# Performance work log

Measured on AMD Instinct MI355X. Metric: run time of the kernel, lower is better.

## Reference

```python
import jax, jax.numpy as jnp
import numpy as np

NEG_INF = -1e30


def setup_inputs() -> dict:
    key = jax.random.key(0)
    kx, km, kq, kk, kv, ko = jax.random.split(key, 6)
    B, D, L = 2, 1024, 2048
    H, DK = 16, 64
    x = jax.random.normal(kx, (B, D, L), dtype=jnp.float32)
    mask = (jax.random.uniform(km, (B, L)) < 0.9).astype(jnp.float32)
    # per-head projection weights, stacked: (H, D, DK); output proj (D, H*DK)==(D, D)
    sq = 1.0 / np.sqrt(D)
    Wq = jax.random.normal(kq, (H, D, DK), dtype=jnp.float32) * sq
    Wk = jax.random.normal(kk, (H, D, DK), dtype=jnp.float32) * sq
    Wv = jax.random.normal(kv, (H, D, DK), dtype=jnp.float32) * sq
    Wo = jax.random.normal(ko, (D, H * DK), dtype=jnp.float32) * sq
    return {"x": x, "mask": mask, "Wq": Wq, "Wk": Wk, "Wv": Wv, "Wo": Wo}


def reference(x, mask, Wq, Wk, Wv, Wo):
    # x: (B, D, L); original transposes to (B, L, D)
    B, D, L = x.shape
    H, _, DK = Wq.shape
    xt = jnp.transpose(x, (0, 2, 1))  # (B, L, D)
    q = jnp.einsum('bld,hdk->bhlk', xt, Wq)
    k = jnp.einsum('bld,hdk->bhlk', xt, Wk)
    v = jnp.einsum('bld,hdk->bhlk', xt, Wv)
    scores = jnp.einsum('bhlk,bhmk->bhlm', q, k) * (1.0 / np.sqrt(DK))
    # masked log-softmax over keys (hmask), squad-style: mask*logit + (1-mask)*-1e30
    hmask = mask[:, None, None, :]  # (B,1,1,Lk)
    masked = hmask * scores + (1.0 - hmask) * NEG_INF
    logp = jax.nn.log_softmax(masked, axis=-1)
    # second softmax over the log-probs, then multiplicative vmask on query dim
    p = jax.nn.softmax(logp, axis=-1) * mask[:, None, :, None]
    heads = jnp.einsum('bhlm,bhmk->bhlk', p, v)  # (B,H,L,DK)
    head = jnp.transpose(heads, (0, 2, 1, 3)).reshape(B, L, H * DK)
    out = jnp.einsum('ble,de->bld', head, Wo)  # matmul(head, Wo) with Wo (D, H*DK)... 
    # NOTE: torch.matmul(head, Wo) treats Wo as (H*DK_in, D_out) only if square; here
    # Wo is (D, H*DK) with D == H*DK, and torch contracts head's last dim with Wo's FIRST dim:
    out = head @ Wo  # (B, L, H*DK) @ (D, H*DK) requires D==H*DK; contracts dim 0 of Wo
    return jnp.transpose(out, (0, 2, 1))  # (B, D, L)


if __name__ == "__main__":
    print(reference(**setup_inputs()).shape)
```

## Files before the change

### kernel.cpp

```cpp
#include <hip/hip_runtime.h>
#include <hip/hip_bf16.h>

typedef unsigned short u16;
typedef unsigned int u32;
typedef unsigned long long u64;
typedef short s8v __attribute__((ext_vector_type(8)));
typedef short s4v __attribute__((ext_vector_type(4)));
typedef __bf16 bfv8 __attribute__((ext_vector_type(8)));
typedef float f4 __attribute__((ext_vector_type(4)));

static constexpr int B = 2, D = 1024, L = 2048, H = 16, DK = 64, E = 1024;
static constexpr float QSCALE = 0.125f * 1.44269504088896340736f;
static constexpr float SMB = -16.0f;
static constexpr float MASKB = -12000.0f;

#define DEV __device__ __forceinline__

DEV u16 f2bf(float f) {
  unsigned int u = __float_as_uint(f);
  u += 0x7FFFu + ((u >> 16) & 1u);
  return (u16)(u >> 16);
}
DEV float fexp2(float x) { return __builtin_amdgcn_exp2f(x); }
DEV u32 pkbf(float a, float b) {
  __hip_bfloat162 h = __float22bfloat162_rn(float2{a, b});
  u32 r;
  __builtin_memcpy(&r, &h, 4);
  return r;
}

DEV f4 mfma16(s4v a, s4v b, f4 c) {
  return __builtin_amdgcn_mfma_f32_16x16x16bf16_1k(a, b, c, 0, 0, 0);
}

#define GLD_LDS16(gp, lp)                                                     \
  __builtin_amdgcn_global_load_lds(                                           \
      (const __attribute__((address_space(1))) void*)(gp),                    \
      (__attribute__((address_space(3))) void*)(lp), 16, 0, 0)

__global__ __launch_bounds__(256) void k_prep(
    const float* __restrict__ x, const float* __restrict__ Wq,
    const float* __restrict__ Wk, const float* __restrict__ Wv,
    const float* __restrict__ Wo, u16* __restrict__ xt, u16* __restrict__ Wt,
    u16* __restrict__ WoT) {
  __shared__ u16 t[64][67];
  const int tid = threadIdx.x;
  const int g = blockIdx.x;
  const float* src;
  u16* dst;
  int sld, dld;
  if (g < 1024) {
    const int b = g >> 9, dt = (g >> 5) & 15, lt = g & 31;
    src = x + ((size_t)b * D + dt * 64) * L + lt * 64;
    sld = L;
    dst = xt + ((size_t)b * L + lt * 64) * D + dt * 64;
    dld = D;
  } else if (g < 1792) {
    const int u = g - 1024;
    const int w = u >> 8, h = (u >> 4) & 15, dt = u & 15;
    const float* Ws = (w == 0) ? Wq : ((w == 1) ? Wk : Wv);
    src = Ws + ((size_t)h * D + dt * 64) * DK;
    sld = DK;
    dst = Wt + ((size_t)(w * H + h) * DK) * D + dt * 64;
    dld = D;
  } else {
    const int v = g - 1792;
    const int et = v >> 4, dt = v & 15;
    src = Wo + ((size_t)et * 64) * D + dt * 64;
    sld = D;
    dst = WoT + ((size_t)dt * 64) * E + et * 64;
    dld = E;
  }
  const int r = tid >> 2, c16 = (tid & 3) * 16;
#pragma unroll
  for (int j = 0; j < 16; j += 4) {
    const f4 v4 = *(const f4*)(src + (size_t)r * sld + c16 + j);
    t[r][c16 + j]     = f2bf(v4[0]);
    t[r][c16 + j + 1] = f2bf(v4[1]);
    t[r][c16 + j + 2] = f2bf(v4[2]);
    t[r][c16 + j + 3] = f2bf(v4[3]);
  }
  __syncthreads();
  s8v o0, o1;
#pragma unroll
  for (int i = 0; i < 8; ++i) {
    o0[i] = (short)t[c16 + i][r];
    o1[i] = (short)t[c16 + 8 + i][r];
  }
  *(s8v*)(dst + (size_t)r * dld + c16)     = o0;
  *(s8v*)(dst + (size_t)r * dld + c16 + 8) = o1;
}

template <int AR>
DEV void gemm_tile(const u16* __restrict__ A, const u16* __restrict__ Bt,
                   int arow0, int brow0, u16* As, u16* Bs,
                   f4 (&acc)[AR / 32][4]) {
  const int tid = threadIdx.x;
  const int wid = tid >> 6, lane = tid & 63;
  const int q = lane >> 4, ln = lane & 15;
  const int wr = wid >> 1, wc = wid & 1;
  const int lrow = lane >> 3;
  const int lc = (lane & 7) ^ lrow;
  const int f0 = (q ^ (ln & 7)) * 8;
  const int f1 = ((q + 4) ^ (ln & 7)) * 8;
  constexpr int MT = AR / 32;

  for (int k0 = 0; k0 < 1024; k0 += 64) {
    __syncthreads();
#pragma unroll
    for (int j = 0; j < AR / 32; ++j) {
      const int rb = wid * (AR / 4) + j * 8;
      GLD_LDS16(A + (size_t)(arow0 + rb + lrow) * 1024 + k0 + lc * 8,
                As + rb * 64);
    }
#pragma unroll
    for (int j = 0; j < 4; ++j) {
      const int rb = wid * 32 + j * 8;
      GLD_LDS16(Bt + (size_t)(brow0 + rb + lrow) * 1024 + k0 + lc * 8,
                Bs + rb * 64);
    }
    __syncthreads();
#pragma unroll
    for (int ks = 0; ks < 2; ++ks) {
      const int fc = ks ? f1 : f0;
      bfv8 af[MT], bf[4];
#pragma unroll
      for (int mt = 0; mt < MT; ++mt)
        af[mt] = *(const bfv8*)(As + (wr * (AR / 2) + mt * 16 + ln) * 64 + fc);
#pragma unroll
      for (int nt = 0; nt < 4; ++nt)
        bf[nt] = *(const bfv8*)(Bs + (wc * 64 + nt * 16 + ln) * 64 + fc);
#pragma unroll
      for (int mt = 0; mt < MT; ++mt)
#pragma unroll
        for (int nt = 0; nt < 4; ++nt)
          acc[mt][nt] = __builtin_amdgcn_mfma_f32_16x16x32_bf16(
              af[mt], bf[nt], acc[mt][nt], 0, 0, 0);
    }
  }
}

__global__ __launch_bounds__(256, 3) void k_qkvg(
    const u16* __restrict__ xt, const u16* __restrict__ Wt,
    u16* __restrict__ Q, u16* __restrict__ K, u16* __restrict__ Vt) {
  __shared__ u16 As[128 * 64];
  __shared__ u16 Bs[128 * 64];
  const int bm = blockIdx.x, bn = blockIdx.y;
  f4 acc[4][4];
#pragma unroll
  for (int mt = 0; mt < 4; ++mt)
#pragma unroll
    for (int nt = 0; nt < 4; ++nt) acc[mt][nt] = (f4){0.f, 0.f, 0.f, 0.f};
  gemm_tile<128>(xt, Wt, bm * 128, bn * 128, As, Bs, acc);

  const int tid = threadIdx.x, wid = tid >> 6, lane = tid & 63;
  const int q = lane >> 4, ln = lane & 15;
  const int wr = wid >> 1, wc = wid & 1;
  const int h2 = bn * 2 + wc;
  const int wsel = h2 >> 4, h = h2 & 15;
  const int b = bm >> 4;
  const int lbase = (bm & 15) * 128 + wr * 64;
  if (wsel == 0) {
    u16* dst = Q + (size_t)(b * H + h) * L * DK;
#pragma unroll
    for (int mt = 0; mt < 4; ++mt)
#pragma unroll
      for (int nt = 0; nt < 4; ++nt)
#pragma unroll
        for (int r = 0; r < 4; ++r)
          dst[(size_t)(lbase + mt * 16 + q * 4 + r) * DK + nt * 16 + ln] =
              f2bf(acc[mt][nt][r] * QSCALE);
  } else if (wsel == 1) {
    u16* dst = K + (size_t)(b * H + h) * L * DK;
#pragma unroll
    for (int mt = 0; mt < 4; ++mt)
#pragma unroll
      for (int nt = 0; nt < 4; ++nt)
#pragma unroll
        for (int r = 0; r < 4; ++r)
          dst[(size_t)(lbase + mt * 16 + q * 4 + r) * DK + nt * 16 + ln] =
              f2bf(acc[mt][nt][r]);
  } else {
    u16* dst = Vt + (size_t)(b * H + h) * DK * L;
#pragma unroll
    for (int mt = 0; mt < 4; ++mt)
#pragma unroll
      for (int nt = 0; nt < 4; ++nt) {
        const u64 pk = (u64)pkbf(acc[mt][nt][0], acc[mt][nt][1]) |
                       ((u64)pkbf(acc[mt][nt][2], acc[mt][nt][3]) << 32);
        *(u64*)(dst + (size_t)(nt * 16 + ln) * L + lbase + mt * 16 + q * 4) =
            pk;
      }
  }
}

__global__ __launch_bounds__(256, 2) void k_attn(
    const u16* __restrict__ Q, const u16* __restrict__ K,
    const u16* __restrict__ Vt, const float* __restrict__ mask,
    u16* __restrict__ Hd) {
  __shared__ u16 kt[2][128 * 64];
  __shared__ u16 vt[2][2][64 * 64];
  __shared__ __align__(16) float mb[L];
  const int h = blockIdx.x, lt = blockIdx.y, b = blockIdx.z;
  const int tid = threadIdx.x;
  const int w = tid >> 6, lane = tid & 63, q = lane >> 4, ln = lane & 15;
  for (int i = tid; i < L; i += 256)
    mb[i] = (mask[(size_t)b * L + i] != 0.0f) ? SMB : MASKB;

  const int bh = b * H + h;
  const u16* Qp = Q + (size_t)bh * L * DK;
  const u16* Kp = K + (size_t)bh * L * DK;
  const u16* Vp = Vt + (size_t)bh * DK * L;
  const int lq = lt * 128 + w * 32;

  bfv8 qf[2][2];
#pragma unroll
  for (int mt = 0; mt < 2; ++mt) {
    qf[mt][0] = *(const bfv8*)(Qp + (size_t)(lq + mt * 16 + ln) * DK + q * 8);
    qf[mt][1] =
        *(const bfv8*)(Qp + (size_t)(lq + mt * 16 + ln) * DK + 32 + q * 8);
  }

  const int lrow = lane >> 3;
  const int lc = (lane & 7) ^ lrow;
  const int fr0 = w * 16 + lrow, fr1 = fr0 + 8;
  const int c0 = (q ^ (ln & 7)) * 8;
  const int c1 = ((q + 4) ^ (ln & 7)) * 8;

  auto stage = [&](int m0, int bufi) {
#pragma unroll
    for (int j = 0; j < 4; ++j) {
      const int rb = w * 32 + j * 8;
      GLD_LDS16(Kp + (size_t)(m0 + rb + lrow) * DK + lc * 8,
                &kt[bufi][rb * 64]);
    }
#pragma unroll
    for (int kh = 0; kh < 2; ++kh) {
      GLD_LDS16(Vp + (size_t)fr0 * L + m0 + kh * 64 + lc * 8,
                &vt[bufi][kh][(w * 16) * 64]);
      GLD_LDS16(Vp + (size_t)fr1 * L + m0 + kh * 64 + lc * 8,
                &vt[bufi][kh][(w * 16 + 8) * 64]);
    }
  };

  f4 ot[2][4];
#pragma unroll
  for (int mt = 0; mt < 2; ++mt)
#pragma unroll
    for (int i = 0; i < 4; ++i) ot[mt][i] = (f4){0.f, 0.f, 0.f, 0.f};
  float lp[2] = {0.f, 0.f};

  stage(0, 0);
  for (int it = 0; it < L / 128; ++it) {
    const int m0 = it * 128;
    __syncthreads();
    if (it + 1 < L / 128) stage(m0 + 128, (it + 1) & 1);
    const int cur = it & 1;
    const u16* ktc = &kt[cur][0];

    s4v pb[2][8];
#pragma unroll
    for (int nt = 0; nt < 8; ++nt) {
      const int krow = nt * 16 + ln;
      const bfv8 kf0 = *(const bfv8*)(ktc + krow * 64 + c0);
      const bfv8 kf1 = *(const bfv8*)(ktc + krow * 64 + c1);
      const f4 mbv = *(const f4*)(mb + m0 + nt * 16 + q * 4);
#pragma unroll
      for (int mt = 0; mt < 2; ++mt) {
        f4 a = mbv;
        a = __builtin_amdgcn_mfma_f32_16x16x32_bf16(kf0, qf[mt][0], a, 0, 0,
                                                    0);
        a = __builtin_amdgcn_mfma_f32_16x16x32_bf16(kf1, qf[mt][1], a, 0, 0,
                                                    0);
        const float p0 = fexp2(a[0]);
        const float p1 = fexp2(a[1]);
        const float p2 = fexp2(a[2]);
        const float p3 = fexp2(a[3]);
        lp[mt] += (p0 + p1) + (p2 + p3);
        const u64 pk = (u64)pkbf(p0, p1) | ((u64)pkbf(p2, p3) << 32);
        pb[mt][nt] = __builtin_bit_cast(s4v, pk);
      }
    }
#pragma unroll
    for (int kh = 0; kh < 2; ++kh) {
      const u16* vtc = &vt[cur][kh][0];
#pragma unroll
      for (int dt = 0; dt < 4; ++dt) {
        const int vrow = dt * 16 + ln;
        const int vbase = vrow * 64 + (q & 1) * 4;
        const int rx = vrow & 7;
        s4v av[4];
#pragma unroll
        for (int kc = 0; kc < 4; ++kc)
          av[kc] =
              *(const s4v*)(vtc + vbase + (((kc * 2 + (q >> 1)) ^ rx) * 8));
#pragma unroll
        for (int kc = 0; kc < 4; ++kc)
#pragma unroll
          for (int mt = 0; mt < 2; ++mt)
            ot[mt][dt] = mfma16(av[kc], pb[mt][kh * 4 + kc], ot[mt][dt]);
      }
    }
  }
#pragma unroll
  for (int mt = 0; mt < 2; ++mt) {
    lp[mt] += __shfl_xor(lp[mt], 16);
    lp[mt] += __shfl_xor(lp[mt], 32);
    const float linv =
        (mb[lq + mt * 16 + ln] > -100.0f) ? (1.0f / lp[mt]) : 0.0f;
#pragma unroll
    for (int dt = 0; dt < 4; ++dt) {
      const u64 pk =
          (u64)pkbf(ot[mt][dt][0] * linv, ot[mt][dt][1] * linv) |
          ((u64)pkbf(ot[mt][dt][2] * linv, ot[mt][dt][3] * linv) << 32);
      *(u64*)(Hd + (size_t)(b * L + lq + mt * 16 + ln) * E + h * DK + dt * 16 +
              q * 4) = pk;
    }
  }
}

__global__ __launch_bounds__(256, 2) void k_projg(const u16* __restrict__ WoT,
                                                  const u16* __restrict__ Hd,
                                                  float* __restrict__ out) {
  __shared__ u16 As[64 * 64];
  __shared__ u16 Bs[128 * 64];
  const int bm = blockIdx.x, bn = blockIdx.y;
  f4 acc[2][4];
#pragma unroll
  for (int mt = 0; mt < 2; ++mt)
#pragma unroll
    for (int nt = 0; nt < 4; ++nt) acc[mt][nt] = (f4){0.f, 0.f, 0.f, 0.f};
  gemm_tile<64>(WoT, Hd, bm * 64, bn * 128, As, Bs, acc);

  const int tid = threadIdx.x, wid = tid >> 6, lane = tid & 63;
  const int q = lane >> 4, ln = lane & 15;
  const int wr = wid >> 1, wc = wid & 1;
#pragma unroll
  for (int mt = 0; mt < 2; ++mt)
#pragma unroll
    for (int nt = 0; nt < 4; ++nt)
#pragma unroll
      for (int r = 0; r < 4; ++r) {
        const int d = bm * 64 + wr * 32 + mt * 16 + q * 4 + r;
        const int n = bn * 128 + wc * 64 + nt * 16 + ln;
        const int bb = n >> 11, l = n & 2047;
        out[((size_t)(bb * D + d)) * L + l] = acc[mt][nt][r];
      }
}

extern "C" void kernel_launch(void* const* d_in, const int* in_sizes, int n_in,
                              void* d_out, int out_size, void* d_ws,
                              size_t ws_size, hipStream_t stream) {
  const float* x    = (const float*)d_in[0];
  const float* mask = (const float*)d_in[1];
  const float* Wq   = (const float*)d_in[2];
  const float* Wk   = (const float*)d_in[3];
  const float* Wv   = (const float*)d_in[4];
  const float* Wo   = (const float*)d_in[5];
  u16* ws = (u16*)d_ws;
  u16* Qws  = ws;
  u16* Kws  = ws + 4194304;
  u16* Vtws = ws + 8388608;
  u16* WoTw = ws + 12582912;
  u16* Wtws = ws + 13631488;
  u16* xtws = ws + 16777216;
  u16* Hdws = ws + 16777216;

  k_prep<<<2048, 256, 0, stream>>>(x, Wq, Wk, Wv, Wo, xtws, Wtws, WoTw);
  k_qkvg<<<dim3(32, 24), 256, 0, stream>>>(xtws, Wtws, Qws, Kws, Vtws);
  k_attn<<<dim3(16, 16, 2), 256, 0, stream>>>(Qws, Kws, Vtws, mask, Hdws);
  k_projg<<<dim3(16, 32), 256, 0, stream>>>(WoTw, Hdws, (float*)d_out);
}
```

Measured before the change: 185.2 us.

## Use 512-thread attention blocks with one query tile per wave and 32-deep PV MFMA

The attention kernel now runs 8 waves of 16 query rows each instead of 4 waves of 32, doubling threads per block while halving per-wave accumulators and registers. K rows are loaded into LDS in a permuted order so the score MFMA output can be repacked directly into 8-element B operands, which lets the P·V product use 16x16x32 MFMAs instead of 16x16x16. The aim is more waves in flight to hide latency and fewer MFMA issues for the PV step. The cost is that each wave reuses its K/V fragments over half as many query rows, so LDS read traffic per FLOP goes up.

```diff
diff --git a/kernel.cpp b/kernel.cpp
--- a/kernel.cpp
+++ b/kernel.cpp
@@ -28,9 +28,18 @@
   __builtin_memcpy(&r, &h, 4);
   return r;
 }
-
-DEV f4 mfma16(s4v a, s4v b, f4 c) {
-  return __builtin_amdgcn_mfma_f32_16x16x16bf16_1k(a, b, c, 0, 0, 0);
+DEV bfv8 cat8(s4v a, s4v b) {
+  s8v r;
+#pragma unroll
+  for (int i = 0; i < 4; ++i) {
+    r[i] = a[i];
+    r[i + 4] = b[i];
+  }
+  return __builtin_bit_cast(bfv8, r);
+}
+DEV int kperm(int kk) {
+  return (kk & 96) | (((kk >> 2) & 3) << 3) | (((kk >> 4) & 1) << 2) |
+         (kk & 3);
 }
 
 #define GLD_LDS16(gp, lp)                                                     \
@@ -194,7 +203,7 @@
   }
 }
 
-__global__ __launch_bounds__(256, 2) void k_attn(
+__global__ __launch_bounds__(512, 4) void k_attn(
     const u16* __restrict__ Q, const u16* __restrict__ K,
     const u16* __restrict__ Vt, const float* __restrict__ mask,
     u16* __restrict__ Hd) {
@@ -204,51 +213,43 @@
   const int h = blockIdx.x, lt = blockIdx.y, b = blockIdx.z;
   const int tid = threadIdx.x;
   const int w = tid >> 6, lane = tid & 63, q = lane >> 4, ln = lane & 15;
-  for (int i = tid; i < L; i += 256)
+  for (int i = tid; i < L; i += 512)
     mb[i] = (mask[(size_t)b * L + i] != 0.0f) ? SMB : MASKB;
 
   const int bh = b * H + h;
   const u16* Qp = Q + (size_t)bh * L * DK;
   const u16* Kp = K + (size_t)bh * L * DK;
   const u16* Vp = Vt + (size_t)bh * DK * L;
-  const int lq = lt * 128 + w * 32;
-
-  bfv8 qf[2][2];
-#pragma unroll
-  for (int mt = 0; mt < 2; ++mt) {
-    qf[mt][0] = *(const bfv8*)(Qp + (size_t)(lq + mt * 16 + ln) * DK + q * 8);
-    qf[mt][1] =
-        *(const bfv8*)(Qp + (size_t)(lq + mt * 16 + ln) * DK + 32 + q * 8);
-  }
+  const int lq = lt * 128 + w * 16;
+
+  bfv8 qf[2];
+  qf[0] = *(const bfv8*)(Qp + (size_t)(lq + ln) * DK + q * 8);
+  qf[1] = *(const bfv8*)(Qp + (size_t)(lq + ln) * DK + 32 + q * 8);
 
   const int lrow = lane >> 3;
   const int lc = (lane & 7) ^ lrow;
-  const int fr0 = w * 16 + lrow, fr1 = fr0 + 8;
   const int c0 = (q ^ (ln & 7)) * 8;
   const int c1 = ((q + 4) ^ (ln & 7)) * 8;
 
   auto stage = [&](int m0, int bufi) {
 #pragma unroll
-    for (int j = 0; j < 4; ++j) {
-      const int rb = w * 32 + j * 8;
-      GLD_LDS16(Kp + (size_t)(m0 + rb + lrow) * DK + lc * 8,
+    for (int j = 0; j < 2; ++j) {
+      const int rb = w * 16 + j * 8;
+      GLD_LDS16(Kp + (size_t)(m0 + kperm(rb + lrow)) * DK + lc * 8,
                 &kt[bufi][rb * 64]);
     }
+    const int fr = w * 8 + lrow;
 #pragma unroll
     for (int kh = 0; kh < 2; ++kh) {
-      GLD_LDS16(Vp + (size_t)fr0 * L + m0 + kh * 64 + lc * 8,
-                &vt[bufi][kh][(w * 16) * 64]);
-      GLD_LDS16(Vp + (size_t)fr1 * L + m0 + kh * 64 + lc * 8,
-                &vt[bufi][kh][(w * 16 + 8) * 64]);
+      GLD_LDS16(Vp + (size_t)fr * L + m0 + kh * 64 + lc * 8,
+                &vt[bufi][kh][(w * 8) * 64]);
     }
   };
 
-  f4 ot[2][4];
-#pragma unroll
-  for (int mt = 0; mt < 2; ++mt)
-#pragma unroll
-    for (int i = 0; i < 4; ++i) ot[mt][i] = (f4){0.f, 0.f, 0.f, 0.f};
-  float lp[2] = {0.f, 0.f};
+  f4 ot[4];
+#pragma unroll
+  for (int i = 0; i < 4; ++i) ot[i] = (f4){0.f, 0.f, 0.f, 0.f};
+  float lp = 0.f;
 
   stage(0, 0);
   for (int it = 0; it < L / 128; ++it) {
@@ -258,28 +259,29 @@
     const int cur = it & 1;
     const u16* ktc = &kt[cur][0];
 
-    s4v pb[2][8];
+    s4v pbe;
+    bfv8 pbx[4];
 #pragma unroll
     for (int nt = 0; nt < 8; ++nt) {
       const int krow = nt * 16 + ln;
       const bfv8 kf0 = *(const bfv8*)(ktc + krow * 64 + c0);
       const bfv8 kf1 = *(const bfv8*)(ktc + krow * 64 + c1);
-      const f4 mbv = *(const f4*)(mb + m0 + nt * 16 + q * 4);
-#pragma unroll
-      for (int mt = 0; mt < 2; ++mt) {
-        f4 a = mbv;
-        a = __builtin_amdgcn_mfma_f32_16x16x32_bf16(kf0, qf[mt][0], a, 0, 0,
-                                                    0);
-        a = __builtin_amdgcn_mfma_f32_16x16x32_bf16(kf1, qf[mt][1], a, 0, 0,
-                                                    0);
-        const float p0 = fexp2(a[0]);
-        const float p1 = fexp2(a[1]);
-        const float p2 = fexp2(a[2]);
-        const float p3 = fexp2(a[3]);
-        lp[mt] += (p0 + p1) + (p2 + p3);
-        const u64 pk = (u64)pkbf(p0, p1) | ((u64)pkbf(p2, p3) << 32);
-        pb[mt][nt] = __builtin_bit_cast(s4v, pk);
-      }
+      const f4 mbv = *(const f4*)(mb + m0 + (nt >> 1) * 32 + (nt & 1) * 4 +
+                                  q * 8);
+      f4 a = mbv;
+      a = __builtin_amdgcn_mfma_f32_16x16x32_bf16(kf0, qf[0], a, 0, 0, 0);
+      a = __builtin_amdgcn_mfma_f32_16x16x32_bf16(kf1, qf[1], a, 0, 0, 0);
+      const float p0 = fexp2(a[0]);
+      const float p1 = fexp2(a[1]);
+      const float p2 = fexp2(a[2]);
+      const float p3 = fexp2(a[3]);
+      lp += (p0 + p1) + (p2 + p3);
+      const u64 pk = (u64)pkbf(p0, p1) | ((u64)pkbf(p2, p3) << 32);
+      const s4v pc = __builtin_bit_cast(s4v, pk);
+      if (nt & 1)
+        pbx[nt >> 1] = cat8(pbe, pc);
+      else
+        pbe = pc;
     }
 #pragma unroll
     for (int kh = 0; kh < 2; ++kh) {
@@ -287,35 +289,26 @@
 #pragma unroll
       for (int dt = 0; dt < 4; ++dt) {
         const int vrow = dt * 16 + ln;
-        const int vbase = vrow * 64 + (q & 1) * 4;
         const int rx = vrow & 7;
-        s4v av[4];
-#pragma unroll
-        for (int kc = 0; kc < 4; ++kc)
-          av[kc] =
-              *(const s4v*)(vtc + vbase + (((kc * 2 + (q >> 1)) ^ rx) * 8));
-#pragma unroll
-        for (int kc = 0; kc < 4; ++kc)
-#pragma unroll
-          for (int mt = 0; mt < 2; ++mt)
-            ot[mt][dt] = mfma16(av[kc], pb[mt][kh * 4 + kc], ot[mt][dt]);
+        const u16* vb = vtc + vrow * 64;
+#pragma unroll
+        for (int g2 = 0; g2 < 2; ++g2) {
+          const bfv8 av = *(const bfv8*)(vb + (((g2 * 4 + q) ^ rx) * 8));
+          ot[dt] = __builtin_amdgcn_mfma_f32_16x16x32_bf16(
+              av, pbx[kh * 2 + g2], ot[dt], 0, 0, 0);
+        }
       }
     }
   }
-#pragma unroll
-  for (int mt = 0; mt < 2; ++mt) {
-    lp[mt] += __shfl_xor(lp[mt], 16);
-    lp[mt] += __shfl_xor(lp[mt], 32);
-    const float linv =
-        (mb[lq + mt * 16 + ln] > -100.0f) ? (1.0f / lp[mt]) : 0.0f;
-#pragma unroll
-    for (int dt = 0; dt < 4; ++dt) {
-      const u64 pk =
-          (u64)pkbf(ot[mt][dt][0] * linv, ot[mt][dt][1] * linv) |
-          ((u64)pkbf(ot[mt][dt][2] * linv, ot[mt][dt][3] * linv) << 32);
-      *(u64*)(Hd + (size_t)(b * L + lq + mt * 16 + ln) * E + h * DK + dt * 16 +
-              q * 4) = pk;
-    }
+  lp += __shfl_xor(lp, 16);
+  lp += __shfl_xor(lp, 32);
+  const float linv = (mb[lq + ln] > -100.0f) ? (1.0f / lp) : 0.0f;
+#pragma unroll
+  for (int dt = 0; dt < 4; ++dt) {
+    const u64 pk = (u64)pkbf(ot[dt][0] * linv, ot[dt][1] * linv) |
+                   ((u64)pkbf(ot[dt][2] * linv, ot[dt][3] * linv) << 32);
+    *(u64*)(Hd + (size_t)(b * L + lq + ln) * E + h * DK + dt * 16 + q * 4) =
+        pk;
   }
 }
 
@@ -368,6 +361,6 @@
 
   k_prep<<<2048, 256, 0, stream>>>(x, Wq, Wk, Wv, Wo, xtws, Wtws, WoTw);
   k_qkvg<<<dim3(32, 24), 256, 0, stream>>>(xtws, Wtws, Qws, Kws, Vtws);
-  k_attn<<<dim3(16, 16, 2), 256, 0, stream>>>(Qws, Kws, Vtws, mask, Hdws);
+  k_attn<<<dim3(16, 16, 2), 512, 0, stream>>>(Qws, Kws, Vtws, mask, Hdws);
   k_projg<<<dim3(16, 32), 256, 0, stream>>>(WoTw, Hdws, (float*)d_out);
 }
```

Measured after the change: 183.1 us. Within noise of the previous version (-1.1%).

## Switch attention kernel to 32x32x16 bf16 MFMA with permuted K staging

Applied to the files above, without the earlier changes.

Rewrites the attention inner loop to use 32x32x16 bf16 MFMAs for both QK^T and PV instead of the 16x16x32 and 16x16x16 variants. K rows are permuted during staging so the 32x32 accumulator layout of P feeds directly as the B operand of the PV MFMA without shuffles. The intent is fewer MFMA issues, fewer LDS fragment loads and a single row-sum reduction per wave. The cost is larger accumulator vectors, which raise register pressure, and a more intricate lane-to-element mapping that has to stay correct.

```diff
diff --git a/kernel.cpp b/kernel.cpp
--- a/kernel.cpp
+++ b/kernel.cpp
@@ -5,9 +5,9 @@
 typedef unsigned int u32;
 typedef unsigned long long u64;
 typedef short s8v __attribute__((ext_vector_type(8)));
-typedef short s4v __attribute__((ext_vector_type(4)));
 typedef __bf16 bfv8 __attribute__((ext_vector_type(8)));
 typedef float f4 __attribute__((ext_vector_type(4)));
+typedef float f16v __attribute__((ext_vector_type(16)));
 
 static constexpr int B = 2, D = 1024, L = 2048, H = 16, DK = 64, E = 1024;
 static constexpr float QSCALE = 0.125f * 1.44269504088896340736f;
@@ -28,9 +28,8 @@
   __builtin_memcpy(&r, &h, 4);
   return r;
 }
-
-DEV f4 mfma16(s4v a, s4v b, f4 c) {
-  return __builtin_amdgcn_mfma_f32_16x16x16bf16_1k(a, b, c, 0, 0, 0);
+DEV int kperm32(int k) {
+  return (k & ~12) | ((k & 4) << 1) | ((k & 8) >> 1);
 }
 
 #define GLD_LDS16(gp, lp)                                                     \
@@ -203,7 +202,8 @@
   __shared__ __align__(16) float mb[L];
   const int h = blockIdx.x, lt = blockIdx.y, b = blockIdx.z;
   const int tid = threadIdx.x;
-  const int w = tid >> 6, lane = tid & 63, q = lane >> 4, ln = lane & 15;
+  const int w = tid >> 6, lane = tid & 63;
+  const int l5 = lane & 31, hi = lane >> 5;
   for (int i = tid; i < L; i += 256)
     mb[i] = (mask[(size_t)b * L + i] != 0.0f) ? SMB : MASKB;
 
@@ -213,42 +213,40 @@
   const u16* Vp = Vt + (size_t)bh * DK * L;
   const int lq = lt * 128 + w * 32;
 
-  bfv8 qf[2][2];
-#pragma unroll
-  for (int mt = 0; mt < 2; ++mt) {
-    qf[mt][0] = *(const bfv8*)(Qp + (size_t)(lq + mt * 16 + ln) * DK + q * 8);
-    qf[mt][1] =
-        *(const bfv8*)(Qp + (size_t)(lq + mt * 16 + ln) * DK + 32 + q * 8);
-  }
+  bfv8 qf[4];
+#pragma unroll
+  for (int st = 0; st < 4; ++st)
+    qf[st] = *(const bfv8*)(Qp + (size_t)(lq + l5) * DK + st * 16 + hi * 8);
 
   const int lrow = lane >> 3;
   const int lc = (lane & 7) ^ lrow;
-  const int fr0 = w * 16 + lrow, fr1 = fr0 + 8;
-  const int c0 = (q ^ (ln & 7)) * 8;
-  const int c1 = ((q + 4) ^ (ln & 7)) * 8;
+  const int x7 = lane & 7;
+  int kpr[4];
+#pragma unroll
+  for (int j = 0; j < 4; ++j) kpr[j] = kperm32(w * 32 + j * 8 + lrow);
 
   auto stage = [&](int m0, int bufi) {
 #pragma unroll
     for (int j = 0; j < 4; ++j) {
-      const int rb = w * 32 + j * 8;
-      GLD_LDS16(Kp + (size_t)(m0 + rb + lrow) * DK + lc * 8,
-                &kt[bufi][rb * 64]);
-    }
-#pragma unroll
-    for (int kh = 0; kh < 2; ++kh) {
-      GLD_LDS16(Vp + (size_t)fr0 * L + m0 + kh * 64 + lc * 8,
-                &vt[bufi][kh][(w * 16) * 64]);
-      GLD_LDS16(Vp + (size_t)fr1 * L + m0 + kh * 64 + lc * 8,
-                &vt[bufi][kh][(w * 16 + 8) * 64]);
-    }
+      GLD_LDS16(Kp + (size_t)(m0 + kpr[j]) * DK + lc * 8,
+                &kt[bufi][(w * 32 + j * 8) * 64]);
+    }
+#pragma unroll
+    for (int kh = 0; kh < 2; ++kh)
+#pragma unroll
+      for (int j = 0; j < 2; ++j) {
+        const int fr = w * 16 + j * 8 + lrow;
+        GLD_LDS16(Vp + (size_t)fr * L + m0 + kh * 64 + lc * 8,
+                  &vt[bufi][kh][(w * 16 + j * 8) * 64]);
+      }
   };
 
-  f4 ot[2][4];
-#pragma unroll
-  for (int mt = 0; mt < 2; ++mt)
-#pragma unroll
-    for (int i = 0; i < 4; ++i) ot[mt][i] = (f4){0.f, 0.f, 0.f, 0.f};
-  float lp[2] = {0.f, 0.f};
+  f16v ot[2];
+#pragma unroll
+  for (int dt = 0; dt < 2; ++dt)
+#pragma unroll
+    for (int i = 0; i < 16; ++i) ot[dt][i] = 0.f;
+  float lp = 0.f;
 
   stage(0, 0);
   for (int it = 0; it < L / 128; ++it) {
@@ -257,66 +255,67 @@
     if (it + 1 < L / 128) stage(m0 + 128, (it + 1) & 1);
     const int cur = it & 1;
     const u16* ktc = &kt[cur][0];
-
-    s4v pb[2][8];
-#pragma unroll
-    for (int nt = 0; nt < 8; ++nt) {
-      const int krow = nt * 16 + ln;
-      const bfv8 kf0 = *(const bfv8*)(ktc + krow * 64 + c0);
-      const bfv8 kf1 = *(const bfv8*)(ktc + krow * 64 + c1);
-      const f4 mbv = *(const f4*)(mb + m0 + nt * 16 + q * 4);
-#pragma unroll
-      for (int mt = 0; mt < 2; ++mt) {
-        f4 a = mbv;
-        a = __builtin_amdgcn_mfma_f32_16x16x32_bf16(kf0, qf[mt][0], a, 0, 0,
-                                                    0);
-        a = __builtin_amdgcn_mfma_f32_16x16x32_bf16(kf1, qf[mt][1], a, 0, 0,
-                                                    0);
-        const float p0 = fexp2(a[0]);
-        const float p1 = fexp2(a[1]);
-        const float p2 = fexp2(a[2]);
-        const float p3 = fexp2(a[3]);
-        lp[mt] += (p0 + p1) + (p2 + p3);
-        const u64 pk = (u64)pkbf(p0, p1) | ((u64)pkbf(p2, p3) << 32);
-        pb[mt][nt] = __builtin_bit_cast(s4v, pk);
-      }
-    }
-#pragma unroll
-    for (int kh = 0; kh < 2; ++kh) {
-      const u16* vtc = &vt[cur][kh][0];
-#pragma unroll
-      for (int dt = 0; dt < 4; ++dt) {
-        const int vrow = dt * 16 + ln;
-        const int vbase = vrow * 64 + (q & 1) * 4;
-        const int rx = vrow & 7;
-        s4v av[4];
-#pragma unroll
-        for (int kc = 0; kc < 4; ++kc)
-          av[kc] =
-              *(const s4v*)(vtc + vbase + (((kc * 2 + (q >> 1)) ^ rx) * 8));
-#pragma unroll
-        for (int kc = 0; kc < 4; ++kc)
-#pragma unroll
-          for (int mt = 0; mt < 2; ++mt)
-            ot[mt][dt] = mfma16(av[kc], pb[mt][kh * 4 + kc], ot[mt][dt]);
-      }
-    }
-  }
-#pragma unroll
-  for (int mt = 0; mt < 2; ++mt) {
-    lp[mt] += __shfl_xor(lp[mt], 16);
-    lp[mt] += __shfl_xor(lp[mt], 32);
-    const float linv =
-        (mb[lq + mt * 16 + ln] > -100.0f) ? (1.0f / lp[mt]) : 0.0f;
-#pragma unroll
-    for (int dt = 0; dt < 4; ++dt) {
+#pragma unroll
+    for (int s = 0; s < 4; ++s) {
+      union {
+        f4 q[4];
+        f16v v;
+      } ai;
+#pragma unroll
+      for (int rq = 0; rq < 4; ++rq)
+        ai.q[rq] = *(const f4*)(mb + m0 + s * 32 + (rq >> 1) * 16 + hi * 8 +
+                                (rq & 1) * 4);
+      f16v a = ai.v;
+#pragma unroll
+      for (int st = 0; st < 4; ++st) {
+        const bfv8 kf = *(const bfv8*)(ktc + (s * 32 + l5) * 64 +
+                                       ((st * 2 + hi) ^ x7) * 8);
+        a = __builtin_amdgcn_mfma_f32_32x32x16_bf16(kf, qf[st], a, 0, 0, 0);
+      }
+      float p[16];
+#pragma unroll
+      for (int i = 0; i < 16; ++i) p[i] = fexp2(a[i]);
+      const float t0 = (p[0] + p[1]) + (p[2] + p[3]);
+      const float t1 = (p[4] + p[5]) + (p[6] + p[7]);
+      const float t2 = (p[8] + p[9]) + (p[10] + p[11]);
+      const float t3 = (p[12] + p[13]) + (p[14] + p[15]);
+      lp += (t0 + t1) + (t2 + t3);
+      union {
+        u32 w4[4];
+        bfv8 v;
+      } pb[2];
+#pragma unroll
+      for (int g = 0; g < 2; ++g)
+#pragma unroll
+        for (int k2 = 0; k2 < 4; ++k2)
+          pb[g].w4[k2] = pkbf(p[g * 8 + k2 * 2], p[g * 8 + k2 * 2 + 1]);
+#pragma unroll
+      for (int g = 0; g < 2; ++g) {
+        const int kg = s * 2 + g;
+        const u16* vtc = &vt[cur][kg >> 2][0];
+        const int cb = (((kg & 3) * 2 + hi) ^ x7) * 8;
+#pragma unroll
+        for (int dt = 0; dt < 2; ++dt) {
+          const bfv8 av = *(const bfv8*)(vtc + (dt * 32 + l5) * 64 + cb);
+          ot[dt] = __builtin_amdgcn_mfma_f32_32x32x16_bf16(av, pb[g].v,
+                                                           ot[dt], 0, 0, 0);
+        }
+      }
+    }
+  }
+  lp += __shfl_xor(lp, 32);
+  const float linv = (mb[lq + l5] > -100.0f) ? (1.0f / lp) : 0.0f;
+#pragma unroll
+  for (int dt = 0; dt < 2; ++dt)
+#pragma unroll
+    for (int rq = 0; rq < 4; ++rq) {
       const u64 pk =
-          (u64)pkbf(ot[mt][dt][0] * linv, ot[mt][dt][1] * linv) |
-          ((u64)pkbf(ot[mt][dt][2] * linv, ot[mt][dt][3] * linv) << 32);
-      *(u64*)(Hd + (size_t)(b * L + lq + mt * 16 + ln) * E + h * DK + dt * 16 +
-              q * 4) = pk;
-    }
-  }
+          (u64)pkbf(ot[dt][rq * 4 + 0] * linv, ot[dt][rq * 4 + 1] * linv) |
+          ((u64)pkbf(ot[dt][rq * 4 + 2] * linv, ot[dt][rq * 4 + 3] * linv)
+           << 32);
+      *(u64*)(Hd + (size_t)(b * L + lq + l5) * E + h * DK + dt * 32 + rq * 8 +
+              hi * 4) = pk;
+    }
 }
 
 __global__ __launch_bounds__(256, 2) void k_projg(const u16* __restrict__ WoT,
```

After: 182.3 us. No clear change (-1.6%).

## Split attention key tiles across two waves per query group and use 16x16x32 MFMA for PV

Applied to the files above, without the earlier changes.

The attention kernel moves to 512 threads, with each pair of waves sharing a query group and splitting each 128-key tile into two halves. K rows are loaded in a permuted order so that the P fragments pair up into 8-wide operands, letting the PV product use the 16x16x32 bf16 MFMA instead of the 16x16x16 one. Partial outputs and row sums from the second wave of each pair are reduced through LDS at the end. s_setprio hints are also added around the MFMA sections. The aim is more waves per block to hide latency and fewer MFMA issues, at the cost of an extra LDS reduction, a barrier, and higher register pressure under the new launch bounds.

```diff
diff --git a/kernel.cpp b/kernel.cpp
--- a/kernel.cpp
+++ b/kernel.cpp
@@ -28,9 +28,18 @@
   __builtin_memcpy(&r, &h, 4);
   return r;
 }
-
-DEV f4 mfma16(s4v a, s4v b, f4 c) {
-  return __builtin_amdgcn_mfma_f32_16x16x16bf16_1k(a, b, c, 0, 0, 0);
+DEV bfv8 cat8(s4v a, s4v b) {
+  s8v r;
+#pragma unroll
+  for (int i = 0; i < 4; ++i) {
+    r[i] = a[i];
+    r[i + 4] = b[i];
+  }
+  return __builtin_bit_cast(bfv8, r);
+}
+DEV int kperm(int kk) {
+  return (kk & 96) | (((kk >> 2) & 3) << 3) | (((kk >> 4) & 1) << 2) |
+         (kk & 3);
 }
 
 #define GLD_LDS16(gp, lp)                                                     \
@@ -194,7 +203,7 @@
   }
 }
 
-__global__ __launch_bounds__(256, 2) void k_attn(
+__global__ __launch_bounds__(512, 4) void k_attn(
     const u16* __restrict__ Q, const u16* __restrict__ K,
     const u16* __restrict__ Vt, const float* __restrict__ mask,
     u16* __restrict__ Hd) {
@@ -204,14 +213,15 @@
   const int h = blockIdx.x, lt = blockIdx.y, b = blockIdx.z;
   const int tid = threadIdx.x;
   const int w = tid >> 6, lane = tid & 63, q = lane >> 4, ln = lane & 15;
-  for (int i = tid; i < L; i += 256)
+  const int wq = w >> 1, wk = w & 1;
+  for (int i = tid; i < L; i += 512)
     mb[i] = (mask[(size_t)b * L + i] != 0.0f) ? SMB : MASKB;
 
   const int bh = b * H + h;
   const u16* Qp = Q + (size_t)bh * L * DK;
   const u16* Kp = K + (size_t)bh * L * DK;
   const u16* Vp = Vt + (size_t)bh * DK * L;
-  const int lq = lt * 128 + w * 32;
+  const int lq = lt * 128 + wq * 32;
 
   bfv8 qf[2][2];
 #pragma unroll
@@ -223,31 +233,34 @@
 
   const int lrow = lane >> 3;
   const int lc = (lane & 7) ^ lrow;
-  const int fr0 = w * 16 + lrow, fr1 = fr0 + 8;
   const int c0 = (q ^ (ln & 7)) * 8;
   const int c1 = ((q + 4) ^ (ln & 7)) * 8;
+  int kpr[2];
+#pragma unroll
+  for (int j = 0; j < 2; ++j) kpr[j] = kperm(w * 16 + j * 8 + lrow);
 
   auto stage = [&](int m0, int bufi) {
 #pragma unroll
-    for (int j = 0; j < 4; ++j) {
-      const int rb = w * 32 + j * 8;
-      GLD_LDS16(Kp + (size_t)(m0 + rb + lrow) * DK + lc * 8,
-                &kt[bufi][rb * 64]);
-    }
+    for (int j = 0; j < 2; ++j) {
+      GLD_LDS16(Kp + (size_t)(m0 + kpr[j]) * DK + lc * 8,
+                &kt[bufi][(w * 16 + j * 8) * 64]);
+    }
+    const int fr = w * 8 + lrow;
 #pragma unroll
     for (int kh = 0; kh < 2; ++kh) {
-      GLD_LDS16(Vp + (size_t)fr0 * L + m0 + kh * 64 + lc * 8,
-                &vt[bufi][kh][(w * 16) * 64]);
-      GLD_LDS16(Vp + (size_t)fr1 * L + m0 + kh * 64 + lc * 8,
-                &vt[bufi][kh][(w * 16 + 8) * 64]);
+      GLD_LDS16(Vp + (size_t)fr * L + m0 + kh * 64 + lc * 8,
+                &vt[bufi][kh][(w * 8) * 64]);
     }
   };
 
-  f4 ot[2][4];
+  union {
+    f4 v;
+    float f[4];
+  } ot[2][4];
 #pragma unroll
   for (int mt = 0; mt < 2; ++mt)
 #pragma unroll
-    for (int i = 0; i < 4; ++i) ot[mt][i] = (f4){0.f, 0.f, 0.f, 0.f};
+    for (int dt = 0; dt < 4; ++dt) ot[mt][dt].v = (f4){0.f, 0.f, 0.f, 0.f};
   float lp[2] = {0.f, 0.f};
 
   stage(0, 0);
@@ -257,64 +270,92 @@
     if (it + 1 < L / 128) stage(m0 + 128, (it + 1) & 1);
     const int cur = it & 1;
     const u16* ktc = &kt[cur][0];
-
-    s4v pb[2][8];
-#pragma unroll
-    for (int nt = 0; nt < 8; ++nt) {
-      const int krow = nt * 16 + ln;
+    const u16* vtc = &vt[cur][wk][0];
+
+    s4v pbe[2];
+    bfv8 pbx[2][2];
+#pragma unroll
+    for (int nt = 0; nt < 4; ++nt) {
+      const int krow = wk * 64 + nt * 16 + ln;
       const bfv8 kf0 = *(const bfv8*)(ktc + krow * 64 + c0);
       const bfv8 kf1 = *(const bfv8*)(ktc + krow * 64 + c1);
-      const f4 mbv = *(const f4*)(mb + m0 + nt * 16 + q * 4);
+      const f4 mbv = *(const f4*)(mb + m0 + wk * 64 + (nt >> 1) * 32 +
+                                  (nt & 1) * 4 + q * 8);
 #pragma unroll
       for (int mt = 0; mt < 2; ++mt) {
         f4 a = mbv;
+        __builtin_amdgcn_s_setprio(1);
         a = __builtin_amdgcn_mfma_f32_16x16x32_bf16(kf0, qf[mt][0], a, 0, 0,
                                                     0);
         a = __builtin_amdgcn_mfma_f32_16x16x32_bf16(kf1, qf[mt][1], a, 0, 0,
                                                     0);
+        __builtin_amdgcn_s_setprio(0);
         const float p0 = fexp2(a[0]);
         const float p1 = fexp2(a[1]);
         const float p2 = fexp2(a[2]);
         const float p3 = fexp2(a[3]);
         lp[mt] += (p0 + p1) + (p2 + p3);
         const u64 pk = (u64)pkbf(p0, p1) | ((u64)pkbf(p2, p3) << 32);
-        pb[mt][nt] = __builtin_bit_cast(s4v, pk);
+        const s4v pc = __builtin_bit_cast(s4v, pk);
+        if (nt & 1)
+          pbx[mt][nt >> 1] = cat8(pbe[mt], pc);
+        else
+          pbe[mt] = pc;
       }
     }
-#pragma unroll
-    for (int kh = 0; kh < 2; ++kh) {
-      const u16* vtc = &vt[cur][kh][0];
+    __builtin_amdgcn_s_setprio(1);
+#pragma unroll
+    for (int g = 0; g < 2; ++g) {
 #pragma unroll
       for (int dt = 0; dt < 4; ++dt) {
         const int vrow = dt * 16 + ln;
-        const int vbase = vrow * 64 + (q & 1) * 4;
-        const int rx = vrow & 7;
-        s4v av[4];
-#pragma unroll
-        for (int kc = 0; kc < 4; ++kc)
-          av[kc] =
-              *(const s4v*)(vtc + vbase + (((kc * 2 + (q >> 1)) ^ rx) * 8));
-#pragma unroll
-        for (int kc = 0; kc < 4; ++kc)
-#pragma unroll
-          for (int mt = 0; mt < 2; ++mt)
-            ot[mt][dt] = mfma16(av[kc], pb[mt][kh * 4 + kc], ot[mt][dt]);
+        const bfv8 av =
+            *(const bfv8*)(vtc + vrow * 64 + (((g * 4 + q) ^ (ln & 7)) * 8));
+#pragma unroll
+        for (int mt = 0; mt < 2; ++mt)
+          ot[mt][dt].v = __builtin_amdgcn_mfma_f32_16x16x32_bf16(
+              av, pbx[mt][g], ot[mt][dt].v, 0, 0, 0);
       }
     }
+    __builtin_amdgcn_s_setprio(0);
   }
 #pragma unroll
   for (int mt = 0; mt < 2; ++mt) {
     lp[mt] += __shfl_xor(lp[mt], 16);
     lp[mt] += __shfl_xor(lp[mt], 32);
-    const float linv =
-        (mb[lq + mt * 16 + ln] > -100.0f) ? (1.0f / lp[mt]) : 0.0f;
-#pragma unroll
-    for (int dt = 0; dt < 4; ++dt) {
-      const u64 pk =
-          (u64)pkbf(ot[mt][dt][0] * linv, ot[mt][dt][1] * linv) |
-          ((u64)pkbf(ot[mt][dt][2] * linv, ot[mt][dt][3] * linv) << 32);
-      *(u64*)(Hd + (size_t)(b * L + lq + mt * 16 + ln) * E + h * DK + dt * 16 +
-              q * 4) = pk;
+  }
+  __syncthreads();
+  float* sOt = (float*)&kt[0][0];
+  float* sLp = (float*)&vt[0][0][0];
+  if (wk) {
+#pragma unroll
+    for (int mt = 0; mt < 2; ++mt) {
+#pragma unroll
+      for (int dt = 0; dt < 4; ++dt)
+        *(f4*)(sOt + ((((wq * 2 + mt) * 4 + dt) * 64) + lane) * 4) =
+            ot[mt][dt].v;
+      sLp[(wq * 2 + mt) * 64 + lane] = lp[mt];
+    }
+  }
+  __syncthreads();
+  if (!wk) {
+#pragma unroll
+    for (int mt = 0; mt < 2; ++mt) {
+#pragma unroll
+      for (int dt = 0; dt < 4; ++dt)
+        ot[mt][dt].v +=
+            *(const f4*)(sOt + ((((wq * 2 + mt) * 4 + dt) * 64) + lane) * 4);
+      lp[mt] += sLp[(wq * 2 + mt) * 64 + lane];
+      const float linv =
+          (mb[lq + mt * 16 + ln] > -100.0f) ? (1.0f / lp[mt]) : 0.0f;
+#pragma unroll
+      for (int dt = 0; dt < 4; ++dt) {
+        const u64 pk =
+            (u64)pkbf(ot[mt][dt].f[0] * linv, ot[mt][dt].f[1] * linv) |
+            ((u64)pkbf(ot[mt][dt].f[2] * linv, ot[mt][dt].f[3] * linv) << 32);
+        *(u64*)(Hd + (size_t)(b * L + lq + mt * 16 + ln) * E + h * DK +
+                dt * 16 + q * 4) = pk;
+      }
     }
   }
 }
@@ -368,6 +409,6 @@
 
   k_prep<<<2048, 256, 0, stream>>>(x, Wq, Wk, Wv, Wo, xtws, Wtws, WoTw);
   k_qkvg<<<dim3(32, 24), 256, 0, stream>>>(xtws, Wtws, Qws, Kws, Vtws);
-  k_attn<<<dim3(16, 16, 2), 256, 0, stream>>>(Qws, Kws, Vtws, mask, Hdws);
+  k_attn<<<dim3(16, 16, 2), 512, 0, stream>>>(Qws, Kws, Vtws, mask, Hdws);
   k_projg<<<dim3(16, 32), 256, 0, stream>>>(WoTw, Hdws, (float*)d_out);
 }
```

After: 174.0 us. 1.06x faster.
